# Kernel optimization log

Hardware: AMD Instinct MI355X
Metric: run time of the kernel (lower is better)

Reference implementation:

```python
import jax, jax.numpy as jnp
import numpy as np

INPUT_DIM = 128
NUM_CLASSES = 10
MAX_DEPTH = 8
HID = 16            # effective_transform_output_dim
TEMP = 1.0
EFF_IN = INPUT_DIM + 2          # root features + parent score + grandparent score
N_INTERNAL = 2 ** MAX_DEPTH - 1  # 255, level-order stacked
N_LEAVES = 2 ** MAX_DEPTH        # 256
BATCH = 32768


def setup_inputs() -> dict:
    key = jax.random.key(0)
    ks = jax.random.split(key, 6)
    x = jax.random.normal(ks[0], (BATCH, INPUT_DIM), jnp.float32)
    path_prob = jnp.ones((BATCH, 1), jnp.float32)
    W1 = jax.random.normal(ks[1], (N_INTERNAL, EFF_IN, HID), jnp.float32) * (1.0 / np.sqrt(EFF_IN))
    b1 = jax.random.normal(ks[2], (N_INTERNAL, HID), jnp.float32) * 0.01
    w2 = jax.random.normal(ks[3], (N_INTERNAL, HID), jnp.float32) * (1.0 / np.sqrt(HID))
    b2 = jax.random.normal(ks[4], (N_INTERNAL,), jnp.float32) * 0.01
    leaf_logits = jax.random.normal(ks[5], (N_LEAVES, NUM_CLASSES), jnp.float32)
    return {"x": x, "path_prob": path_prob, "W1": W1, "b1": b1,
            "w2": w2, "b2": b2, "leaf_logits": leaf_logits}


def reference(x, path_prob, W1, b1, w2, b2, leaf_logits):
    """Depth-batched soft binary tree: all 2^d nodes at depth d are processed
    as one batched GEMM instead of the original sequential recursion."""
    B = x.shape[0]
    pp = path_prob                              # [B, n_nodes_at_depth]
    parent = jnp.zeros((B, 1), x.dtype)         # parent decision scores (0 => unused at depth 0)
    grandp = jnp.zeros((B, 1), x.dtype)         # grandparent scores (0 => unused at depth 0,1)
    for d in range(MAX_DEPTH):
        lo, hi = 2 ** d - 1, 2 ** (d + 1) - 1   # level-order slice of this depth's nodes
        W1d = W1[lo:hi]                          # [N, EFF_IN, HID]
        # concat([x, parent, grandparent]) @ W1d without materializing the concat
        h = jnp.einsum('be,neh->bnh', x, W1d[:, :INPUT_DIM, :])
        h = h + parent[:, :, None] * W1d[None, :, INPUT_DIM, :]
        h = h + grandp[:, :, None] * W1d[None, :, INPUT_DIM + 1, :]
        t = jax.nn.relu(h + b1[lo:hi][None])                       # [B, N, HID]
        score = jnp.einsum('bnh,nh->bn', t, w2[lo:hi]) + b2[lo:hi][None]  # [B, N]
        p = jax.nn.sigmoid(score / TEMP)
        n = pp.shape[1]
        # children: left gets p, right gets 1-p; level-order interleave
        pp = jnp.stack([pp * p, pp * (1.0 - p)], axis=-1).reshape(B, 2 * n)
        grandp = jnp.repeat(parent, 2, axis=1)   # child's grandparent = node's parent
        parent = jnp.repeat(score, 2, axis=1)    # child's parent_out = this node's raw score
    # leaves: sum_n path_prob[:, n] * output_logits[n]
    return jnp.einsum('bn,nc->bc', pp, leaf_logits)
```

## Files before the change

kernel.cpp:

```cpp
#include <hip/hip_runtime.h>
#include <math.h>

namespace {

typedef __attribute__((ext_vector_type(8))) __fp16 f16x8;
typedef __attribute__((ext_vector_type(4))) float f32x4;

constexpr int IN_DIM = 128;
constexpr int EFF    = 130 * 16;
constexpr int NODES  = 255;
constexpr int TS     = 64;
constexpr int BLOCK  = 256;
constexpr int NC     = 10;

__global__ __launch_bounds__(256) void prep_w1(const float* __restrict__ W1,
                                               f16x8* __restrict__ wfrag) {
    __shared__ float xs[IN_DIM * 16];
    const int n = blockIdx.x, tid = threadIdx.x;
    const float4* src = (const float4*)(W1 + (size_t)n * EFF);
    ((float4*)xs)[tid]       = src[tid];
    ((float4*)xs)[tid + 256] = src[tid + 256];
    __syncthreads();
    const int l = tid & 63, t = tid >> 6;
    const int k0 = t * 32 + (l >> 4) * 8, hid = l & 15;
    f16x8 hv;
    #pragma unroll
    for (int j = 0; j < 8; ++j)
        hv[j] = (__fp16)xs[(k0 + j) * 16 + hid];
    wfrag[(n * 4 + t) * 64 + l] = hv;
}

__device__ __forceinline__ void loadW(const f16x8* __restrict__ wfrag, int n, int l,
                                      f16x8 (&w)[4]) {
    const f16x8* wp = wfrag + (size_t)n * 256 + l;
    #pragma unroll
    for (int t = 0; t < 4; ++t) w[t] = wp[t * 64];
}

__device__ __forceinline__ void mfma16(const f16x8 (&w)[4], const f16x8 (&xh)[4][4],
                                       f32x4 (&acc)[4]) {
    #pragma unroll
    for (int t = 0; t < 4; ++t)
        #pragma unroll
        for (int mt = 0; mt < 4; ++mt)
            acc[mt] = __builtin_amdgcn_mfma_f32_16x16x32_f16(w[t], xh[t][mt], acc[mt], 0, 0, 0);
}

#define COMP4(v, r) ((r == 0) ? v.x : (r == 1) ? v.y : (r == 2) ? v.z : v.w)

__device__ __forceinline__ float epi_score(
    const f32x4 (&acc)[4], const float4& w2q, const float4& wpq, const float4& wgq,
    const float (&par)[4], const float (&gp)[4], float b2v, int quad)
{
    float p4[4];
    #pragma unroll
    for (int mt = 0; mt < 4; ++mt) {
        float ts = 0.0f;
        #pragma unroll
        for (int r = 0; r < 4; ++r) {
            const float wpr = COMP4(wpq, r);
            const float wgr = COMP4(wgq, r);
            const float w2r = COMP4(w2q, r);
            const float h = fmaf(par[mt], wpr, fmaf(gp[mt], wgr, acc[mt][r]));
            ts = fmaf(fmaxf(h, 0.0f), w2r, ts);
        }
        p4[mt] = ts;
    }
    const bool hiQ = (quad & 2) != 0;
    const bool loQ = (quad & 1) != 0;
    const float a  = hiQ ? p4[2] : p4[0];
    const float b  = hiQ ? p4[3] : p4[1];
    const float sa = hiQ ? p4[0] : p4[2];
    const float sb = hiQ ? p4[1] : p4[3];
    const float uA = a + __shfl_xor(sa, 32);
    const float uB = b + __shfl_xor(sb, 32);
    const float k  = loQ ? uB : uA;
    const float s  = loQ ? uA : uB;
    return k + __shfl_xor(s, 16) + b2v;
}

__global__ __launch_bounds__(BLOCK) __attribute__((amdgpu_waves_per_eu(2)))
void tree_mfma(
    const float* __restrict__ x, const float* __restrict__ path_prob,
    const float* __restrict__ W1, const float* __restrict__ b1,
    const float* __restrict__ w2, const float* __restrict__ b2,
    const float* __restrict__ leaf_logits,
    const f16x8* __restrict__ wfrag,
    float* __restrict__ out)
{
    __shared__ float pp[128][TS];
    __shared__ float scbuf[127][TS];

    const int tid  = threadIdx.x;
    const int wv   = tid >> 6, l = tid & 63;
    const int quad = l >> 4,   col = l & 15;
    const int s0   = blockIdx.x * TS;

    if (tid < TS) pp[0][tid] = path_prob[s0 + tid];

    f16x8 xh[4][4];
    #pragma unroll
    for (int t = 0; t < 4; ++t)
        #pragma unroll
        for (int mt = 0; mt < 4; ++mt) {
            const float* xp = x + (size_t)(s0 + mt * 16 + col) * IN_DIM + t * 32 + quad * 8;
            float4 v0 = ((const float4*)xp)[0];
            float4 v1 = ((const float4*)xp)[1];
            float vv[8] = {v0.x, v0.y, v0.z, v0.w, v1.x, v1.y, v1.z, v1.w};
            f16x8 hv;
            #pragma unroll
            for (int j = 0; j < 8; ++j) hv[j] = (__fp16)vv[j];
            xh[t][mt] = hv;
        }

    #pragma unroll
    for (int d = 0; d < 3; ++d) {
        const int nd = 1 << d;
        const int stride = 128 >> d, half = 64 >> d;
        if (wv < nd) {
            const int n = nd - 1 + wv;
            f16x8 w[4];
            loadW(wfrag, n, l, w);
            const float4 b1q = ((const float4*)(b1 + n * 16))[quad];
            const float4 w2q = ((const float4*)(w2 + n * 16))[quad];
            const float4 wpq = ((const float4*)(W1 + (size_t)n * EFF + 128 * 16))[quad];
            const float4 wgq = ((const float4*)(W1 + (size_t)n * EFF + 129 * 16))[quad];
            const float  b2v = b2[n];
            float par[4], gp[4];
            #pragma unroll
            for (int mt = 0; mt < 4; ++mt) {
                const int scol = mt * 16 + col;
                par[mt] = (d >= 1) ? scbuf[(nd >> 1) - 1 + (wv >> 1)][scol] : 0.0f;
                gp[mt]  = (d >= 2) ? scbuf[(nd >> 2) - 1 + (wv >> 2)][scol] : 0.0f;
            }
            const int   slot = wv * stride;
            const float ppar = pp[slot][l];

            f32x4 binit = {b1q.x, b1q.y, b1q.z, b1q.w};
            f32x4 acc[4] = {binit, binit, binit, binit};
            mfma16(w, xh, acc);

            const float sv = epi_score(acc, w2q, wpq, wgq, par, gp, b2v, quad);
            scbuf[nd - 1 + wv][l] = sv;
            const float p = 1.0f / (1.0f + __expf(-sv));
            pp[slot][l]        = ppar * p;
            pp[slot + half][l] = ppar * (1.0f - p);
        }
        if (d < 2) __syncthreads();
    }

    bool   havePrev = false;
    f32x4  cAccA[4], cAccB[4];
    float4 cW2A, cW2B, cWpA, cWpB, cWgA, cWgB;
    float  cB2A = 0.f, cB2B = 0.f, cPparA = 0.f, cPparB = 0.f;
    float  cPar[4], cGp[4];
    int    cScw = 0, cSlotA = 0, cSlotB = 0, cHalf = 0;

    for (int d = 3; d < 7; ++d) {
        const int nd = 1 << d;
        const int stride = 128 >> d, half = 64 >> d;
        const int base = nd - 1, scPo = (nd >> 1) - 1, scP2o = (nd >> 2) - 1;
        const int ilo = wv * (nd >> 3), ihi = ilo + (nd >> 3);
        for (int i = ilo; i < ihi; ++i) {
            const int nA = base + 2 * i, nB = nA + 1;

            f16x8 wA[4], wB[4];
            loadW(wfrag, nA, l, wA);
            loadW(wfrag, nB, l, wB);
            const float4 b1A = ((const float4*)(b1 + nA * 16))[quad];
            const float4 b1B = ((const float4*)(b1 + nB * 16))[quad];

            if (havePrev) {
                const float svA = epi_score(cAccA, cW2A, cWpA, cWgA, cPar, cGp, cB2A, quad);
                const float svB = epi_score(cAccB, cW2B, cWpB, cWgB, cPar, cGp, cB2B, quad);
                scbuf[cScw][l]     = svA;
                scbuf[cScw + 1][l] = svB;
                const float pA = 1.0f / (1.0f + __expf(-svA));
                const float pB = 1.0f / (1.0f + __expf(-svB));
                pp[cSlotA][l]         = cPparA * pA;
                pp[cSlotA + cHalf][l] = cPparA * (1.0f - pA);
                pp[cSlotB][l]         = cPparB * pB;
                pp[cSlotB + cHalf][l] = cPparB * (1.0f - pB);
            }

            const float4 w2A = ((const float4*)(w2 + nA * 16))[quad];
            const float4 w2B = ((const float4*)(w2 + nB * 16))[quad];
            const float4 wpA = ((const float4*)(W1 + (size_t)nA * EFF + 128 * 16))[quad];
            const float4 wpB = ((const float4*)(W1 + (size_t)nB * EFF + 128 * 16))[quad];
            const float4 wgA = ((const float4*)(W1 + (size_t)nA * EFF + 129 * 16))[quad];
            const float4 wgB = ((const float4*)(W1 + (size_t)nB * EFF + 129 * 16))[quad];
            const float  b2A = b2[nA], b2B = b2[nB];
            float par[4], gp[4];
            #pragma unroll
            for (int mt = 0; mt < 4; ++mt) {
                const int scol = mt * 16 + col;
                par[mt] = scbuf[scPo + i][scol];
                gp[mt]  = scbuf[scP2o + (i >> 1)][scol];
            }
            const int   slotA = (2 * i) * stride, slotB = slotA + stride;
            const float pparA = pp[slotA][l], pparB = pp[slotB][l];

            f32x4 iAi = {b1A.x, b1A.y, b1A.z, b1A.w};
            f32x4 iBi = {b1B.x, b1B.y, b1B.z, b1B.w};
            f32x4 accA[4] = {iAi, iAi, iAi, iAi};
            f32x4 accB[4] = {iBi, iBi, iBi, iBi};
            mfma16(wA, xh, accA);
            mfma16(wB, xh, accB);

            #pragma unroll
            for (int mt = 0; mt < 4; ++mt) { cAccA[mt] = accA[mt]; cAccB[mt] = accB[mt]; }
            cW2A = w2A; cW2B = w2B; cWpA = wpA; cWpB = wpB; cWgA = wgA; cWgB = wgB;
            cB2A = b2A; cB2B = b2B; cPparA = pparA; cPparB = pparB;
            #pragma unroll
            for (int mt = 0; mt < 4; ++mt) { cPar[mt] = par[mt]; cGp[mt] = gp[mt]; }
            cScw = base + 2 * i; cSlotA = slotA; cSlotB = slotB; cHalf = half;
            havePrev = true;
        }
    }
    if (havePrev) {
        const float svA = epi_score(cAccA, cW2A, cWpA, cWgA, cPar, cGp, cB2A, quad);
        const float svB = epi_score(cAccB, cW2B, cWpB, cWgB, cPar, cGp, cB2B, quad);
        scbuf[cScw][l]     = svA;
        scbuf[cScw + 1][l] = svB;
        const float pA = 1.0f / (1.0f + __expf(-svA));
        const float pB = 1.0f / (1.0f + __expf(-svB));
        pp[cSlotA][l]         = cPparA * pA;
        pp[cSlotA + cHalf][l] = cPparA * (1.0f - pA);
        pp[cSlotB][l]         = cPparB * pB;
        pp[cSlotB + cHalf][l] = cPparB * (1.0f - pB);
    }

    float oacc[NC];
    #pragma unroll
    for (int c = 0; c < NC; ++c) oacc[c] = 0.0f;
    {
        bool hp = false;
        int  cPl = 0;
        const int ilo = wv * 16, ihi = ilo + 16;
        for (int i = ilo; i < ihi; ++i) {
            const int nA = 127 + 2 * i, nB = nA + 1;

            f16x8 wA[4], wB[4];
            loadW(wfrag, nA, l, wA);
            loadW(wfrag, nB, l, wB);
            const float4 b1A = ((const float4*)(b1 + nA * 16))[quad];
            const float4 b1B = ((const float4*)(b1 + nB * 16))[quad];

            if (hp) {
                const float4* lp4 = (const float4*)(leaf_logits + (size_t)(4 * cPl) * NC);
                float4 lv[10];
                #pragma unroll
                for (int q = 0; q < 10; ++q) lv[q] = lp4[q];
                const float* lf = (const float*)lv;

                const float svA = epi_score(cAccA, cW2A, cWpA, cWgA, cPar, cGp, cB2A, quad);
                const float svB = epi_score(cAccB, cW2B, cWpB, cWgB, cPar, cGp, cB2B, quad);
                const float pA = 1.0f / (1.0f + __expf(-svA));
                const float pB = 1.0f / (1.0f + __expf(-svB));
                const float pLA = cPparA * pA, pRA = cPparA * (1.0f - pA);
                const float pLB = cPparB * pB, pRB = cPparB * (1.0f - pB);
                #pragma unroll
                for (int c = 0; c < NC; ++c)
                    oacc[c] = fmaf(pLA, lf[c], fmaf(pRA, lf[NC + c], oacc[c]));
                #pragma unroll
                for (int c = 0; c < NC; ++c)
                    oacc[c] = fmaf(pLB, lf[2 * NC + c], fmaf(pRB, lf[3 * NC + c], oacc[c]));
            }

            const float4 w2A = ((const float4*)(w2 + nA * 16))[quad];
            const float4 w2B = ((const float4*)(w2 + nB * 16))[quad];
            const float4 wpA = ((const float4*)(W1 + (size_t)nA * EFF + 128 * 16))[quad];
            const float4 wpB = ((const float4*)(W1 + (size_t)nB * EFF + 128 * 16))[quad];
            const float4 wgA = ((const float4*)(W1 + (size_t)nA * EFF + 129 * 16))[quad];
            const float4 wgB = ((const float4*)(W1 + (size_t)nB * EFF + 129 * 16))[quad];
            const float  b2A = b2[nA], b2B = b2[nB];
            float par[4], gp[4];
            #pragma unroll
            for (int mt = 0; mt < 4; ++mt) {
                const int scol = mt * 16 + col;
                par[mt] = scbuf[63 + i][scol];
                gp[mt]  = scbuf[31 + (i >> 1)][scol];
            }
            const float pparA = pp[2 * i][l], pparB = pp[2 * i + 1][l];

            f32x4 iAi = {b1A.x, b1A.y, b1A.z, b1A.w};
            f32x4 iBi = {b1B.x, b1B.y, b1B.z, b1B.w};
            f32x4 accA[4] = {iAi, iAi, iAi, iAi};
            f32x4 accB[4] = {iBi, iBi, iBi, iBi};
            mfma16(wA, xh, accA);
            mfma16(wB, xh, accB);

            #pragma unroll
            for (int mt = 0; mt < 4; ++mt) { cAccA[mt] = accA[mt]; cAccB[mt] = accB[mt]; }
            cW2A = w2A; cW2B = w2B; cWpA = wpA; cWpB = wpB; cWgA = wgA; cWgB = wgB;
            cB2A = b2A; cB2B = b2B; cPparA = pparA; cPparB = pparB;
            #pragma unroll
            for (int mt = 0; mt < 4; ++mt) { cPar[mt] = par[mt]; cGp[mt] = gp[mt]; }
            cPl = i;
            hp = true;
        }
        if (hp) {
            const float4* lp4 = (const float4*)(leaf_logits + (size_t)(4 * cPl) * NC);
            float4 lv[10];
            #pragma unroll
            for (int q = 0; q < 10; ++q) lv[q] = lp4[q];
            const float* lf = (const float*)lv;

            const float svA = epi_score(cAccA, cW2A, cWpA, cWgA, cPar, cGp, cB2A, quad);
            const float svB = epi_score(cAccB, cW2B, cWpB, cWgB, cPar, cGp, cB2B, quad);
            const float pA = 1.0f / (1.0f + __expf(-svA));
            const float pB = 1.0f / (1.0f + __expf(-svB));
            const float pLA = cPparA * pA, pRA = cPparA * (1.0f - pA);
            const float pLB = cPparB * pB, pRB = cPparB * (1.0f - pB);
            #pragma unroll
            for (int c = 0; c < NC; ++c)
                oacc[c] = fmaf(pLA, lf[c], fmaf(pRA, lf[NC + c], oacc[c]));
            #pragma unroll
            for (int c = 0; c < NC; ++c)
                oacc[c] = fmaf(pLB, lf[2 * NC + c], fmaf(pRB, lf[3 * NC + c], oacc[c]));
        }
    }

    __syncthreads();
    {
        float* red = &scbuf[0][0];
        #pragma unroll
        for (int c = 0; c < NC; ++c)
            red[(wv * 64 + l) * NC + c] = oacc[c];
    }
    __syncthreads();
    {
        const float* red = &scbuf[0][0];
        for (int i = tid; i < TS * NC; i += BLOCK) {
            float v = red[i] + red[640 + i] + red[1280 + i] + red[1920 + i];
            out[(size_t)s0 * NC + i] = v;
        }
    }
}

}

extern "C" void kernel_launch(void* const* d_in, const int* in_sizes, int n_in,
                              void* d_out, int out_size, void* d_ws, size_t ws_size,
                              hipStream_t stream) {
    const float* x           = (const float*)d_in[0];
    const float* path_prob   = (const float*)d_in[1];
    const float* W1          = (const float*)d_in[2];
    const float* b1          = (const float*)d_in[3];
    const float* w2          = (const float*)d_in[4];
    const float* b2          = (const float*)d_in[5];
    const float* leaf_logits = (const float*)d_in[6];
    float* out = (float*)d_out;

    const int batch = in_sizes[0] / IN_DIM;
    f16x8* wfrag = (f16x8*)d_ws;

    hipLaunchKernelGGL(prep_w1, dim3(NODES), dim3(256), 0, stream, W1, wfrag);
    hipLaunchKernelGGL(tree_mfma, dim3(batch / TS), dim3(BLOCK), 0, stream,
                       x, path_prob, W1, b1, w2, b2, leaf_logits, wfrag, out);
}
```

Baseline: 135.5 us.

## Compute top tree levels redundantly per wave with shuffles, removing barriers

Every wave now computes depths 0-2 itself. Each wave handles the root, its depth-1 ancestor and its own depth-2 node, and passes parent and grandparent scores through wave shuffles instead of shared memory. This removes the two early __syncthreads and the idle waves in the first levels, at the cost of redundant MFMA work for the root and depth-1 nodes. It also adds s_setprio around the MFMA sequences and makes the wave index scalar with readfirstlane.

```diff
diff --git a/kernel.cpp b/kernel.cpp
--- a/kernel.cpp
+++ b/kernel.cpp
@@ -92,11 +92,10 @@
     __shared__ float scbuf[127][TS];
 
     const int tid  = threadIdx.x;
-    const int wv   = tid >> 6, l = tid & 63;
+    const int wv   = __builtin_amdgcn_readfirstlane(tid >> 6);
+    const int l    = tid & 63;
     const int quad = l >> 4,   col = l & 15;
     const int s0   = blockIdx.x * TS;
-
-    if (tid < TS) pp[0][tid] = path_prob[s0 + tid];
 
     f16x8 xh[4][4];
     #pragma unroll
@@ -113,40 +112,79 @@
             xh[t][mt] = hv;
         }
 
-    #pragma unroll
-    for (int d = 0; d < 3; ++d) {
-        const int nd = 1 << d;
-        const int stride = 128 >> d, half = 64 >> d;
-        if (wv < nd) {
-            const int n = nd - 1 + wv;
-            f16x8 w[4];
-            loadW(wfrag, n, l, w);
-            const float4 b1q = ((const float4*)(b1 + n * 16))[quad];
-            const float4 w2q = ((const float4*)(w2 + n * 16))[quad];
-            const float4 wpq = ((const float4*)(W1 + (size_t)n * EFF + 128 * 16))[quad];
-            const float4 wgq = ((const float4*)(W1 + (size_t)n * EFF + 129 * 16))[quad];
-            const float  b2v = b2[n];
-            float par[4], gp[4];
-            #pragma unroll
-            for (int mt = 0; mt < 4; ++mt) {
-                const int scol = mt * 16 + col;
-                par[mt] = (d >= 1) ? scbuf[(nd >> 1) - 1 + (wv >> 1)][scol] : 0.0f;
-                gp[mt]  = (d >= 2) ? scbuf[(nd >> 2) - 1 + (wv >> 2)][scol] : 0.0f;
-            }
-            const int   slot = wv * stride;
-            const float ppar = pp[slot][l];
-
-            f32x4 binit = {b1q.x, b1q.y, b1q.z, b1q.w};
-            f32x4 acc[4] = {binit, binit, binit, binit};
-            mfma16(w, xh, acc);
-
-            const float sv = epi_score(acc, w2q, wpq, wgq, par, gp, b2v, quad);
-            scbuf[nd - 1 + wv][l] = sv;
-            const float p = 1.0f / (1.0f + __expf(-sv));
-            pp[slot][l]        = ppar * p;
-            pp[slot + half][l] = ppar * (1.0f - p);
-        }
-        if (d < 2) __syncthreads();
+    const int j1 = wv >> 1;
+    float sc0, sc1, sc2;
+    const float z4[4] = {0.0f, 0.0f, 0.0f, 0.0f};
+
+    {
+        f16x8 w[4];
+        loadW(wfrag, 0, l, w);
+        const float4 b1q = ((const float4*)(b1))[quad];
+        const float4 w2q = ((const float4*)(w2))[quad];
+        const float4 wpq = ((const float4*)(W1 + 128 * 16))[quad];
+        const float4 wgq = ((const float4*)(W1 + 129 * 16))[quad];
+        const float  b2v = b2[0];
+        f32x4 binit = {b1q.x, b1q.y, b1q.z, b1q.w};
+        f32x4 acc[4] = {binit, binit, binit, binit};
+        __builtin_amdgcn_s_setprio(1);
+        mfma16(w, xh, acc);
+        __builtin_amdgcn_s_setprio(0);
+        sc0 = epi_score(acc, w2q, wpq, wgq, z4, z4, b2v, quad);
+    }
+    const float pp0 = path_prob[s0 + l];
+    const float p0  = 1.0f / (1.0f + __expf(-sc0));
+    const float pp1 = (j1 == 0) ? pp0 * p0 : pp0 * (1.0f - p0);
+
+    float pp2;
+    {
+        const int n = 1 + j1;
+        f16x8 w[4];
+        loadW(wfrag, n, l, w);
+        const float4 b1q = ((const float4*)(b1 + n * 16))[quad];
+        const float4 w2q = ((const float4*)(w2 + n * 16))[quad];
+        const float4 wpq = ((const float4*)(W1 + (size_t)n * EFF + 128 * 16))[quad];
+        const float4 wgq = ((const float4*)(W1 + (size_t)n * EFF + 129 * 16))[quad];
+        const float  b2v = b2[n];
+        float par[4];
+        #pragma unroll
+        for (int mt = 0; mt < 4; ++mt) par[mt] = __shfl(sc0, mt * 16 + col);
+        f32x4 binit = {b1q.x, b1q.y, b1q.z, b1q.w};
+        f32x4 acc[4] = {binit, binit, binit, binit};
+        __builtin_amdgcn_s_setprio(1);
+        mfma16(w, xh, acc);
+        __builtin_amdgcn_s_setprio(0);
+        sc1 = epi_score(acc, w2q, wpq, wgq, par, z4, b2v, quad);
+        const float p = 1.0f / (1.0f + __expf(-sc1));
+        pp2 = ((wv & 1) == 0) ? pp1 * p : pp1 * (1.0f - p);
+    }
+
+    {
+        const int n = 3 + wv;
+        f16x8 w[4];
+        loadW(wfrag, n, l, w);
+        const float4 b1q = ((const float4*)(b1 + n * 16))[quad];
+        const float4 w2q = ((const float4*)(w2 + n * 16))[quad];
+        const float4 wpq = ((const float4*)(W1 + (size_t)n * EFF + 128 * 16))[quad];
+        const float4 wgq = ((const float4*)(W1 + (size_t)n * EFF + 129 * 16))[quad];
+        const float  b2v = b2[n];
+        float par[4], gp[4];
+        #pragma unroll
+        for (int mt = 0; mt < 4; ++mt) {
+            const int scol = mt * 16 + col;
+            par[mt] = __shfl(sc1, scol);
+            gp[mt]  = __shfl(sc0, scol);
+        }
+        f32x4 binit = {b1q.x, b1q.y, b1q.z, b1q.w};
+        f32x4 acc[4] = {binit, binit, binit, binit};
+        __builtin_amdgcn_s_setprio(1);
+        mfma16(w, xh, acc);
+        __builtin_amdgcn_s_setprio(0);
+        sc2 = epi_score(acc, w2q, wpq, wgq, par, gp, b2v, quad);
+        const float p = 1.0f / (1.0f + __expf(-sc2));
+        pp[32 * wv][l]      = pp2 * p;
+        pp[32 * wv + 16][l] = pp2 * (1.0f - p);
+        scbuf[1 + j1][l] = sc1;
+        scbuf[3 + wv][l] = sc2;
     }
 
     bool   havePrev = false;
@@ -204,8 +242,10 @@
             f32x4 iBi = {b1B.x, b1B.y, b1B.z, b1B.w};
             f32x4 accA[4] = {iAi, iAi, iAi, iAi};
             f32x4 accB[4] = {iBi, iBi, iBi, iBi};
+            __builtin_amdgcn_s_setprio(1);
             mfma16(wA, xh, accA);
             mfma16(wB, xh, accB);
+            __builtin_amdgcn_s_setprio(0);
 
             #pragma unroll
             for (int mt = 0; mt < 4; ++mt) { cAccA[mt] = accA[mt]; cAccB[mt] = accB[mt]; }
@@ -287,8 +327,10 @@
             f32x4 iBi = {b1B.x, b1B.y, b1B.z, b1B.w};
             f32x4 accA[4] = {iAi, iAi, iAi, iAi};
             f32x4 accB[4] = {iBi, iBi, iBi, iBi};
+            __builtin_amdgcn_s_setprio(1);
             mfma16(wA, xh, accA);
             mfma16(wB, xh, accB);
+            __builtin_amdgcn_s_setprio(0);
 
             #pragma unroll
             for (int mt = 0; mt < 4; ++mt) { cAccA[mt] = accA[mt]; cAccB[mt] = accB[mt]; }
```

Result: faster. 128.3 us (median of 3 runs) (-5.3%).
